# Kernel tuning notes

Measured on AMD Instinct MI355X. Metric: run time of the kernel, lower is better.

The kernel has to match this reference:

```python
import jax, jax.numpy as jnp
import numpy as np

B, N3, N4, DIM, HEADS, MLP = 256, 256, 64, 512, 8, 2048
EPS = 1e-5

def _sinusoid(n_position, d_hid):
    pos = np.arange(n_position)[:, None].astype(np.float64)
    i = np.arange(d_hid)[None, :]
    angle = pos / np.power(10000.0, 2 * (i // 2) / d_hid)
    tab = np.empty((n_position, d_hid))
    tab[:, 0::2] = np.sin(angle[:, 0::2])
    tab[:, 1::2] = np.cos(angle[:, 1::2])
    return jnp.asarray(tab[None], dtype=jnp.float32)  # [1, n, d]

def _ln(x, g, b):
    m = x.mean(-1, keepdims=True)
    v = ((x - m) ** 2).mean(-1, keepdims=True)
    return (x - m) / jnp.sqrt(v + EPS) * g + b

def setup_inputs() -> dict:
    key = jax.random.key(0)
    ks = jax.random.split(key, 12)
    s = 0.02
    d = {
        'f3': jax.random.normal(ks[0], (B, N3, DIM), jnp.float32),
        'f4': jax.random.normal(ks[1], (B, N4, DIM), jnp.float32),
        'pos3': _sinusoid(N3, DIM),
        'pos4': _sinusoid(N4, DIM),
        'ln1_g': jnp.ones((DIM,), jnp.float32), 'ln1_b': jnp.zeros((DIM,), jnp.float32),
        'ln2_g': jnp.ones((DIM,), jnp.float32), 'ln2_b': jnp.zeros((DIM,), jnp.float32),
        'ln3_g': jnp.ones((DIM,), jnp.float32), 'ln3_b': jnp.zeros((DIM,), jnp.float32),
        'Wq': jax.random.normal(ks[2], (DIM, DIM), jnp.float32) * s, 'bq': jnp.zeros((DIM,), jnp.float32),
        'Wk': jax.random.normal(ks[3], (DIM, DIM), jnp.float32) * s, 'bk': jnp.zeros((DIM,), jnp.float32),
        'Wv': jax.random.normal(ks[4], (DIM, DIM), jnp.float32) * s, 'bv': jnp.zeros((DIM,), jnp.float32),
        'Wr': jax.random.normal(ks[5], (DIM, DIM), jnp.float32) * s, 'br': jnp.zeros((DIM,), jnp.float32),
        'W1': jax.random.normal(ks[6], (DIM, MLP), jnp.float32) * s, 'b1': jnp.zeros((MLP,), jnp.float32),
        'W2': jax.random.normal(ks[7], (MLP, DIM), jnp.float32) * s, 'b2': jnp.zeros((DIM,), jnp.float32),
    }
    return d

def reference(f3, f4, pos3, pos4, ln1_g, ln1_b, ln2_g, ln2_b, ln3_g, ln3_b,
              Wq, bq, Wk, bk, Wv, bv, Wr, br, W1, b1, W2, b2):
    dk = DIM // HEADS
    f3n = _ln(f3, ln1_g, ln1_b)
    f4n = _ln(f4, ln2_g, ln2_b)
    # projections (dropout=0 -> eval mode)
    q = (f3n + pos3) @ Wq + bq  # [B,N3,D]
    k = (f4n + pos4) @ Wk + bk  # [B,N4,D]
    v = f4n @ Wv + bv           # [B,N4,D]
    # split heads along channel dim (contiguous slices == reshape with head major)
    q = q.reshape(B, N3, HEADS, dk).transpose(0, 2, 3, 1)  # [B,H,dk,N3]
    k = k.reshape(B, N4, HEADS, dk).transpose(0, 2, 3, 1)  # [B,H,dk,N4]
    v = v.reshape(B, N4, HEADS, dk).transpose(0, 2, 3, 1)  # [B,H,dv,N4]
    q = jax.nn.softmax(q, axis=2)  # softmax over head channels
    k = jax.nn.softmax(k, axis=3)  # softmax over key positions
    context = jnp.einsum('bhkn,bhvn->bhkv', k, v)          # [B,H,dk,dv]
    att = jnp.einsum('bhkv,bhkn->bhvn', context, q)        # [B,H,dv,N3]
    att = att.transpose(0, 3, 1, 2).reshape(B, N3, DIM)    # concat heads -> [B,N3,D]
    f3 = f3 + (att @ Wr + br)
    h = _ln(f3, ln3_g, ln3_b)
    h = jax.nn.gelu(h @ W1 + b1, approximate=False) @ W2 + b2
    return f3 + h
```

## Files before the change

kernel.cpp:

```cpp
#include <hip/hip_runtime.h>
#include <hip/hip_bf16.h>

typedef __attribute__((ext_vector_type(8))) short short8v;
typedef __attribute__((ext_vector_type(4))) float f32x4;
typedef __hip_bfloat16 bf16;

#define BDIM 512
#define NHEADS 8
#define DK 64
#define NBATCH 256
#define NN3 256
#define NN4 64
#define NMLP 2048

#define GLOAD_LDS16(g, l)                                                  \
  __builtin_amdgcn_global_load_lds(                                        \
      (const __attribute__((address_space(1))) void*)(g),                  \
      (__attribute__((address_space(3))) void*)(l), 16, 0, 0)

__device__ __forceinline__ float bf2f(short s) {
  union { short u[2]; float f; } cv;
  cv.u[0] = 0; cv.u[1] = s;
  return cv.f;
}
__device__ __forceinline__ short f2bf(float x) {
  bf16 h = __float2bfloat16(x);
  return *reinterpret_cast<short*>(&h);
}

__global__ __launch_bounds__(256) void convt_kernel(
    const float* __restrict__ W, bf16* __restrict__ Wt, int K, int N) {
  __shared__ float tile[32][33];
  int bx = blockIdx.x * 32, by = blockIdx.y * 32;
  int tx = threadIdx.x, ty = threadIdx.y;
#pragma unroll
  for (int j = 0; j < 32; j += 8)
    tile[ty + j][tx] = W[(size_t)(by + ty + j) * N + bx + tx];
  __syncthreads();
#pragma unroll
  for (int j = 0; j < 32; j += 8)
    Wt[(size_t)(bx + ty + j) * K + by + tx] = __float2bfloat16(tile[tx][ty + j]);
}

__global__ __launch_bounds__(256) void ln_kernel(
    const float* __restrict__ x, const float* __restrict__ g,
    const float* __restrict__ beta, const float* __restrict__ pos, int nmod,
    bf16* __restrict__ out1, bf16* __restrict__ out2, bf16* __restrict__ raw) {
  int w = threadIdx.x >> 6, lane = threadIdx.x & 63;
  int row = blockIdx.x * 4 + w;
  int c0 = lane * 8;
  const float* xr = x + (size_t)row * BDIM + c0;
  float4 v0 = *(const float4*)xr;
  float4 v1 = *(const float4*)(xr + 4);
  float f[8] = {v0.x, v0.y, v0.z, v0.w, v1.x, v1.y, v1.z, v1.w};
  float s = 0.f, sq = 0.f;
#pragma unroll
  for (int i = 0; i < 8; i++) {
    s += f[i];
    sq += f[i] * f[i];
  }
#pragma unroll
  for (int o = 1; o <= 32; o <<= 1) {
    s += __shfl_xor(s, o);
    sq += __shfl_xor(sq, o);
  }
  float mean = s * (1.f / BDIM);
  float var = sq * (1.f / BDIM) - mean * mean;
  float rstd = rsqrtf(var + 1e-5f);
  float4 g0 = *(const float4*)(g + c0);
  float4 g1 = *(const float4*)(g + c0 + 4);
  float4 b0 = *(const float4*)(beta + c0);
  float4 b1 = *(const float4*)(beta + c0 + 4);
  float gg[8] = {g0.x, g0.y, g0.z, g0.w, g1.x, g1.y, g1.z, g1.w};
  float bb[8] = {b0.x, b0.y, b0.z, b0.w, b1.x, b1.y, b1.z, b1.w};
  float pv[8] = {};
  if (pos) {
    int n = row % nmod;
    const float* pr = pos + (size_t)n * BDIM + c0;
    float4 p0 = *(const float4*)pr;
    float4 p1 = *(const float4*)(pr + 4);
    pv[0] = p0.x; pv[1] = p0.y; pv[2] = p0.z; pv[3] = p0.w;
    pv[4] = p1.x; pv[5] = p1.y; pv[6] = p1.z; pv[7] = p1.w;
  }
  short8v o1, o2, rw;
#pragma unroll
  for (int i = 0; i < 8; i++) {
    float nv = (f[i] - mean) * rstd * gg[i] + bb[i];
    o1[i] = f2bf(nv + pv[i]);
    o2[i] = f2bf(nv);
    rw[i] = f2bf(f[i]);
  }
  size_t ob = (size_t)row * BDIM + c0;
  *(short8v*)(out1 + ob) = o1;
  if (out2) *(short8v*)(out2 + ob) = o2;
  if (raw) *(short8v*)(raw + ob) = rw;
}

__global__ __launch_bounds__(256) void lnb_kernel(
    const bf16* __restrict__ x, const float* __restrict__ g,
    const float* __restrict__ beta, bf16* __restrict__ out) {
  int w = threadIdx.x >> 6, lane = threadIdx.x & 63;
  int row = blockIdx.x * 4 + w;
  int c0 = lane * 8;
  short8v v = *(const short8v*)(x + (size_t)row * BDIM + c0);
  float f[8];
  float s = 0.f, sq = 0.f;
#pragma unroll
  for (int i = 0; i < 8; i++) {
    f[i] = bf2f(v[i]);
    s += f[i];
    sq += f[i] * f[i];
  }
#pragma unroll
  for (int o = 1; o <= 32; o <<= 1) {
    s += __shfl_xor(s, o);
    sq += __shfl_xor(sq, o);
  }
  float mean = s * (1.f / BDIM);
  float var = sq * (1.f / BDIM) - mean * mean;
  float rstd = rsqrtf(var + 1e-5f);
  float4 g0 = *(const float4*)(g + c0);
  float4 g1 = *(const float4*)(g + c0 + 4);
  float4 b0 = *(const float4*)(beta + c0);
  float4 b1 = *(const float4*)(beta + c0 + 4);
  float gg[8] = {g0.x, g0.y, g0.z, g0.w, g1.x, g1.y, g1.z, g1.w};
  float bb[8] = {b0.x, b0.y, b0.z, b0.w, b1.x, b1.y, b1.z, b1.w};
  short8v o1;
#pragma unroll
  for (int i = 0; i < 8; i++) o1[i] = f2bf((f[i] - mean) * rstd * gg[i] + bb[i]);
  *(short8v*)(out + (size_t)row * BDIM + c0) = o1;
}

template <int EPI>
__global__ __launch_bounds__(512, 4) void gemm_kernel(
    const bf16* __restrict__ X, const bf16* __restrict__ Wt,
    const float* __restrict__ bias, const void* __restrict__ src, void* outp,
    int K, int ldx, int ldw, int N, int gridX) {
  extern __shared__ bf16 lds[];

  int nwg = gridDim.x;
  int cpx = nwg >> 3;
  int bid = blockIdx.x;
  int nb = (bid & 7) * cpx + (bid >> 3);
  int bx = nb % gridX, by = nb / gridX;
  int row0 = by * 128, col0 = bx * 256;

  int t = threadIdx.x, w = t >> 6, lane = t & 63;
  int wr = w >> 2, wc = w & 3;
  int r16 = lane & 15, kg = lane >> 4;
  int srow = lane >> 2;
  int scol = ((lane & 3) ^ (srow & 3)) * 8;

  const bf16* gA0 = X + (size_t)(row0 + w * 16 + srow) * ldx + scol;
  const bf16* gB0 = Wt + (size_t)(col0 + w * 32 + srow) * ldw + scol;

  f32x4 acc[4][4] = {};

  auto stage = [&](int kt, int buf) {
    bf16* base = lds + buf * 12288;
    int ke = kt << 5;
    GLOAD_LDS16(gA0 + ke, base + w * 512 + lane * 8);
    GLOAD_LDS16(gB0 + ke, base + 4096 + w * 1024 + lane * 8);
    GLOAD_LDS16(gB0 + ke + (size_t)16 * ldw,
                base + 4096 + w * 1024 + 512 + lane * 8);
  };

  auto compute = [&](int buf) {
    const char* base = (const char*)(lds + buf * 12288);
    int cc = ((kg ^ (r16 & 3)) << 4);
    short8v a[4], b[4];
#pragma unroll
    for (int m = 0; m < 4; m++)
      a[m] = *(const short8v*)(base + (wr * 64 + m * 16 + r16) * 64 + cc);
#pragma unroll
    for (int n = 0; n < 4; n++)
      b[n] = *(const short8v*)(base + 8192 + (wc * 64 + n * 16 + r16) * 64 + cc);
#pragma unroll
    for (int m = 0; m < 4; m++)
#pragma unroll
      for (int n = 0; n < 4; n++)
        acc[m][n] =
            __builtin_amdgcn_mfma_f32_16x16x32_bf16(a[m], b[n], acc[m][n], 0, 0, 0);
  };

  int NT = K >> 5;
  stage(0, 0);
  stage(1, 1);
  for (int tt = 0; tt < NT; tt++) {
    if (tt < NT - 1)
      asm volatile("s_waitcnt vmcnt(3)" ::: "memory");
    else
      asm volatile("s_waitcnt vmcnt(0)" ::: "memory");
    __builtin_amdgcn_s_barrier();
    asm volatile("" ::: "memory");
    compute(tt & 1);
    asm volatile("" ::: "memory");
    __builtin_amdgcn_s_barrier();
    asm volatile("" ::: "memory");
    if (tt + 2 < NT) stage(tt + 2, tt & 1);
  }

#pragma unroll
  for (int n = 0; n < 4; n++) {
    int col = col0 + wc * 64 + n * 16 + r16;
    float bv = bias ? bias[col] : 0.f;
#pragma unroll
    for (int m = 0; m < 4; m++)
#pragma unroll
      for (int r = 0; r < 4; r++) {
        int row = row0 + wr * 64 + m * 16 + kg * 4 + r;
        size_t o = (size_t)row * N + col;
        float val = acc[m][n][r] + bv;
        if (EPI == 0) {
          ((bf16*)outp)[o] = __float2bfloat16(val);
        } else if (EPI == 1) {
          float z = 1.5957691f * val * (1.f + 0.044715f * val * val);
          float gl = val / (1.f + __expf(-z));
          ((bf16*)outp)[o] = __float2bfloat16(gl);
        } else if (EPI == 3) {
          ((bf16*)outp)[o] = __float2bfloat16(bf2f(((const short*)src)[o]) + val);
        } else {
          ((float*)outp)[o] = bf2f(((const short*)src)[o]) + val;
        }
      }
  }
}

__global__ __launch_bounds__(256) void ctx_kernel(
    const bf16* __restrict__ kproj, const bf16* __restrict__ vbuf,
    bf16* __restrict__ ctxT) {
  int bh = blockIdx.x;
  int b = bh >> 3, h = bh & 7;
  __shared__ bf16 lk[NN4][DK], lv[NN4][DK];
  int t = threadIdx.x;
#pragma unroll
  for (int i = 0; i < 16; i++) {
    int idx = i * 256 + t;
    int n = idx >> 6, c = idx & 63;
    size_t gaddr = (size_t)b * NN4 * BDIM + (size_t)n * BDIM + h * DK + c;
    lk[n][c] = kproj[gaddr];
    lv[n][c] = vbuf[gaddr];
  }
  __syncthreads();
  if (t < 64) {
    int c = t;
    float e[NN4];
    float m = -1e30f;
#pragma unroll
    for (int n = 0; n < NN4; n++) {
      e[n] = bf2f(*(short*)&lk[n][c]);
      m = fmaxf(m, e[n]);
    }
    float s = 0.f;
#pragma unroll
    for (int n = 0; n < NN4; n++) {
      e[n] = __expf(e[n] - m);
      s += e[n];
    }
    float inv = 1.f / s;
#pragma unroll
    for (int n = 0; n < NN4; n++) lk[n][c] = __float2bfloat16(e[n] * inv);
  }
  __syncthreads();
  int vc = t >> 2;
  int kc0 = (t & 3) * 16;
  float acc[16] = {};
  for (int n = 0; n < NN4; n++) {
    float vv = __bfloat162float(lv[n][vc]);
#pragma unroll
    for (int i = 0; i < 16; i++)
      acc[i] += vv * __bfloat162float(lk[n][kc0 + i]);
  }
  size_t o = (size_t)bh * 4096 + (size_t)vc * 64 + kc0;
#pragma unroll
  for (int i = 0; i < 16; i++) ctxT[o + i] = __float2bfloat16(acc[i]);
}

__global__ __launch_bounds__(256) void att_kernel(
    const bf16* __restrict__ qproj, const bf16* __restrict__ ctxT,
    bf16* __restrict__ att) {
  int bh = blockIdx.x;
  int b = bh >> 3, h = bh & 7;
  int t = threadIdx.x, w = t >> 6, lane = t & 63;
  int r16 = lane & 15, kg = lane >> 4;
  f32x4 acc[4][4] = {};
  const bf16* qb = qproj + (size_t)b * NN3 * BDIM + h * DK;
  const bf16* cb = ctxT + (size_t)bh * 4096;
  short8v bb[2][4];
#pragma unroll
  for (int kt = 0; kt < 2; kt++)
#pragma unroll
    for (int ni = 0; ni < 4; ni++)
      bb[kt][ni] = *(const short8v*)(cb + (ni * 16 + r16) * 64 + kt * 32 + kg * 8);
#pragma unroll
  for (int mi = 0; mi < 4; mi++) {
    int rrow = w * 64 + mi * 16 + r16;
    short8v a0 = *(const short8v*)(qb + (size_t)rrow * BDIM + kg * 8);
    short8v a1 = *(const short8v*)(qb + (size_t)rrow * BDIM + 32 + kg * 8);
    float f[16];
#pragma unroll
    for (int i = 0; i < 8; i++) {
      f[i] = bf2f(a0[i]);
      f[8 + i] = bf2f(a1[i]);
    }
    float m = f[0];
#pragma unroll
    for (int i = 1; i < 16; i++) m = fmaxf(m, f[i]);
    m = fmaxf(m, __shfl_xor(m, 16));
    m = fmaxf(m, __shfl_xor(m, 32));
    float s = 0.f;
#pragma unroll
    for (int i = 0; i < 16; i++) {
      f[i] = __expf(f[i] - m);
      s += f[i];
    }
    s += __shfl_xor(s, 16);
    s += __shfl_xor(s, 32);
    float inv = 1.f / s;
    short8v A0, A1;
#pragma unroll
    for (int i = 0; i < 8; i++) {
      A0[i] = f2bf(f[i] * inv);
      A1[i] = f2bf(f[8 + i] * inv);
    }
#pragma unroll
    for (int ni = 0; ni < 4; ni++) {
      acc[mi][ni] = __builtin_amdgcn_mfma_f32_16x16x32_bf16(A0, bb[0][ni], acc[mi][ni], 0, 0, 0);
      acc[mi][ni] = __builtin_amdgcn_mfma_f32_16x16x32_bf16(A1, bb[1][ni], acc[mi][ni], 0, 0, 0);
    }
  }
#pragma unroll
  for (int mi = 0; mi < 4; mi++)
#pragma unroll
    for (int ni = 0; ni < 4; ni++)
#pragma unroll
      for (int r = 0; r < 4; r++) {
        int row = w * 64 + mi * 16 + kg * 4 + r;
        int col = ni * 16 + r16;
        att[(size_t)(b * NN3 + row) * BDIM + h * DK + col] =
            __float2bfloat16(acc[mi][ni][r]);
      }
}

extern "C" void kernel_launch(void* const* d_in, const int* in_sizes, int n_in,
                              void* d_out, int out_size, void* d_ws, size_t ws_size,
                              hipStream_t stream) {
  const float* f3 = (const float*)d_in[0];
  const float* f4 = (const float*)d_in[1];
  const float* pos3 = (const float*)d_in[2];
  const float* pos4 = (const float*)d_in[3];
  const float* ln1_g = (const float*)d_in[4];
  const float* ln1_b = (const float*)d_in[5];
  const float* ln2_g = (const float*)d_in[6];
  const float* ln2_b = (const float*)d_in[7];
  const float* ln3_g = (const float*)d_in[8];
  const float* ln3_b = (const float*)d_in[9];
  const float* Wq = (const float*)d_in[10];
  const float* bq = (const float*)d_in[11];
  const float* Wk = (const float*)d_in[12];
  const float* bk = (const float*)d_in[13];
  const float* Wv = (const float*)d_in[14];
  const float* bv = (const float*)d_in[15];
  const float* Wr = (const float*)d_in[16];
  const float* br = (const float*)d_in[17];
  const float* W1 = (const float*)d_in[18];
  const float* b1 = (const float*)d_in[19];
  const float* W2 = (const float*)d_in[20];
  const float* b2 = (const float*)d_in[21];
  float* out = (float*)d_out;

  const int M3 = NBATCH * NN3;
  const int M4 = NBATCH * NN4;
  const int MC = M3 / 2;

  char* ws = (char*)d_ws;
  size_t off = 0;
  auto alloc = [&](size_t bytes) {
    size_t r = off;
    off = (off + bytes + 255) & ~(size_t)255;
    return r;
  };
  size_t oWqt = alloc((size_t)BDIM * BDIM * 2);
  size_t oWkt = alloc((size_t)BDIM * BDIM * 2);
  size_t oWvt = alloc((size_t)BDIM * BDIM * 2);
  size_t oWrt = alloc((size_t)BDIM * BDIM * 2);
  size_t oW1t = alloc((size_t)BDIM * NMLP * 2);
  size_t oW2t = alloc((size_t)BDIM * NMLP * 2);
  size_t oXQ = alloc((size_t)M3 * BDIM * 2);
  size_t oXK = alloc((size_t)M4 * BDIM * 2);
  size_t oXV = alloc((size_t)M4 * BDIM * 2);
  size_t oQF = alloc((size_t)M3 * BDIM * 2);
  size_t oKF = alloc((size_t)M4 * BDIM * 2);
  size_t oVF = alloc((size_t)M4 * BDIM * 2);
  size_t oF3B = alloc((size_t)M3 * BDIM * 2);
  size_t oCT = alloc((size_t)NBATCH * NHEADS * DK * DK * 2);
  size_t oH1 = alloc((size_t)MC * NMLP * 2);
  (void)ws_size;

  bf16* Wqt = (bf16*)(ws + oWqt);
  bf16* Wkt = (bf16*)(ws + oWkt);
  bf16* Wvt = (bf16*)(ws + oWvt);
  bf16* Wrt = (bf16*)(ws + oWrt);
  bf16* W1t = (bf16*)(ws + oW1t);
  bf16* W2t = (bf16*)(ws + oW2t);
  bf16* XQ = (bf16*)(ws + oXQ);
  bf16* XK = (bf16*)(ws + oXK);
  bf16* XV = (bf16*)(ws + oXV);
  bf16* QF = (bf16*)(ws + oQF);
  bf16* KF = (bf16*)(ws + oKF);
  bf16* VF = (bf16*)(ws + oVF);
  bf16* F3B = (bf16*)(ws + oF3B);
  bf16* CT = (bf16*)(ws + oCT);
  bf16* H1 = (bf16*)(ws + oH1);
  bf16* ATT = XQ;
  bf16* F3O = QF;
  bf16* YN = XQ;

  hipFuncSetAttribute((const void*)gemm_kernel<0>,
                      hipFuncAttributeMaxDynamicSharedMemorySize, 49152);
  hipFuncSetAttribute((const void*)gemm_kernel<1>,
                      hipFuncAttributeMaxDynamicSharedMemorySize, 49152);
  hipFuncSetAttribute((const void*)gemm_kernel<3>,
                      hipFuncAttributeMaxDynamicSharedMemorySize, 49152);
  hipFuncSetAttribute((const void*)gemm_kernel<4>,
                      hipFuncAttributeMaxDynamicSharedMemorySize, 49152);

  convt_kernel<<<dim3(BDIM / 32, BDIM / 32), dim3(32, 8), 0, stream>>>(Wq, Wqt, BDIM, BDIM);
  convt_kernel<<<dim3(BDIM / 32, BDIM / 32), dim3(32, 8), 0, stream>>>(Wk, Wkt, BDIM, BDIM);
  convt_kernel<<<dim3(BDIM / 32, BDIM / 32), dim3(32, 8), 0, stream>>>(Wv, Wvt, BDIM, BDIM);
  convt_kernel<<<dim3(BDIM / 32, BDIM / 32), dim3(32, 8), 0, stream>>>(Wr, Wrt, BDIM, BDIM);
  convt_kernel<<<dim3(NMLP / 32, BDIM / 32), dim3(32, 8), 0, stream>>>(W1, W1t, BDIM, NMLP);
  convt_kernel<<<dim3(BDIM / 32, NMLP / 32), dim3(32, 8), 0, stream>>>(W2, W2t, NMLP, BDIM);

  ln_kernel<<<M3 / 4, 256, 0, stream>>>(f3, ln1_g, ln1_b, pos3, NN3, XQ, nullptr, F3B);
  ln_kernel<<<M4 / 4, 256, 0, stream>>>(f4, ln2_g, ln2_b, pos4, NN4, XK, XV, nullptr);

  gemm_kernel<0><<<(BDIM / 256) * (M3 / 128), 512, 49152, stream>>>(
      XQ, Wqt, bq, nullptr, QF, BDIM, BDIM, BDIM, BDIM, BDIM / 256);
  gemm_kernel<0><<<(BDIM / 256) * (M4 / 128), 512, 49152, stream>>>(
      XK, Wkt, bk, nullptr, KF, BDIM, BDIM, BDIM, BDIM, BDIM / 256);
  gemm_kernel<0><<<(BDIM / 256) * (M4 / 128), 512, 49152, stream>>>(
      XV, Wvt, bv, nullptr, VF, BDIM, BDIM, BDIM, BDIM, BDIM / 256);

  ctx_kernel<<<NBATCH * NHEADS, 256, 0, stream>>>(KF, VF, CT);
  att_kernel<<<NBATCH * NHEADS, 256, 0, stream>>>(QF, CT, ATT);

  gemm_kernel<3><<<(BDIM / 256) * (M3 / 128), 512, 49152, stream>>>(
      ATT, Wrt, br, F3B, F3O, BDIM, BDIM, BDIM, BDIM, BDIM / 256);

  lnb_kernel<<<M3 / 4, 256, 0, stream>>>(F3O, ln3_g, ln3_b, YN);

  for (int c = 0; c < 2; c++) {
    const bf16* Yc = YN + (size_t)c * MC * BDIM;
    const bf16* Fc = F3O + (size_t)c * MC * BDIM;
    float* outc = out + (size_t)c * MC * BDIM;
    gemm_kernel<1><<<(NMLP / 256) * (MC / 128), 512, 49152, stream>>>(
        Yc, W1t, b1, nullptr, H1, BDIM, BDIM, BDIM, NMLP, NMLP / 256);
    gemm_kernel<4><<<(BDIM / 256) * (MC / 128), 512, 49152, stream>>>(
        H1, W2t, b2, Fc, outc, NMLP, NMLP, NMLP, BDIM, BDIM / 256);
  }
}
```

Measured before the change: 848.0 us.

## Replace GEMM with 256x256 tile, BK=64, eight-phase interleaved load/MFMA pipeline

Swaps the 128x256-tile, BK=32 GEMM for a 256x256-tile, BK=64 kernel with 128KB double-buffered LDS. The kernel splits each k-step into four sub-phases that interleave global-to-LDS staging with MFMA work. The aim is more reuse per loaded byte and better overlap of loads with compute. The cost is fewer workgroups per CU (occupancy 2), a doubled accumulator register footprint, and half as many tiles, which may underfill the GPU on the small K/V projections.

New measurement: 806.3 us. 4.9% less time.

```diff
diff --git a/kernel.cpp b/kernel.cpp
--- a/kernel.cpp
+++ b/kernel.cpp
@@ -131,84 +131,111 @@
   *(short8v*)(out + (size_t)row * BDIM + c0) = o1;
 }
 
+#define VM4 asm volatile("s_waitcnt vmcnt(4)" ::: "memory")
+#define VM2 asm volatile("s_waitcnt vmcnt(2)" ::: "memory")
+#define VM0 asm volatile("s_waitcnt vmcnt(0)" ::: "memory")
+#define BARR                          \
+  __builtin_amdgcn_s_barrier();       \
+  asm volatile("" ::: "memory")
+
+#define PH_A(SLOT, MH)                                                        \
+  _Pragma("unroll") for (int mq = 0; mq < 4; mq++) {                          \
+    _Pragma("unroll") for (int ks = 0; ks < 2; ks++) {                        \
+      int rl = wr * 64 + mq * 16 + r16;                                       \
+      ac[mq][ks] = *(const short8v*)((const char*)lds + (SLOT)*65536 +        \
+          (MH)*16384 + rl * 128 + ((((ks << 2) + kg) ^ (rl & 7)) << 4));      \
+    }                                                                          \
+  }
+#define PH_B(SLOT, NH)                                                        \
+  _Pragma("unroll") for (int nq = 0; nq < 2; nq++) {                          \
+    _Pragma("unroll") for (int ks = 0; ks < 2; ks++) {                        \
+      int cl = wc * 16 + nq * 64 + r16;                                       \
+      bb[nq][ks] = *(const short8v*)((const char*)lds + (SLOT)*65536 +        \
+          32768 + (NH)*16384 + cl * 128 + ((((ks << 2) + kg) ^ (cl & 7)) << 4)); \
+    }                                                                          \
+  }
+#define PH_MMA(MH, NH)                                                        \
+  _Pragma("unroll") for (int mq = 0; mq < 4; mq++)                            \
+  _Pragma("unroll") for (int nq = 0; nq < 2; nq++)                            \
+  _Pragma("unroll") for (int ks = 0; ks < 2; ks++)                            \
+    acc[(MH)*4 + mq][(NH)*2 + nq] = __builtin_amdgcn_mfma_f32_16x16x32_bf16(  \
+        ac[mq][ks], bb[nq][ks], acc[(MH)*4 + mq][(NH)*2 + nq], 0, 0, 0);
+
 template <int EPI>
-__global__ __launch_bounds__(512, 4) void gemm_kernel(
+__global__ __launch_bounds__(512, 2) void gemm8p_kernel(
     const bf16* __restrict__ X, const bf16* __restrict__ Wt,
     const float* __restrict__ bias, const void* __restrict__ src, void* outp,
     int K, int ldx, int ldw, int N, int gridX) {
   extern __shared__ bf16 lds[];
 
-  int nwg = gridDim.x;
-  int cpx = nwg >> 3;
-  int bid = blockIdx.x;
+  int nwg = gridDim.x, cpx = nwg >> 3, bid = blockIdx.x;
   int nb = (bid & 7) * cpx + (bid >> 3);
   int bx = nb % gridX, by = nb / gridX;
-  int row0 = by * 128, col0 = bx * 256;
+  int row0 = by * 256, col0 = bx * 256;
 
   int t = threadIdx.x, w = t >> 6, lane = t & 63;
   int wr = w >> 2, wc = w & 3;
   int r16 = lane & 15, kg = lane >> 4;
-  int srow = lane >> 2;
-  int scol = ((lane & 3) ^ (srow & 3)) * 8;
-
-  const bf16* gA0 = X + (size_t)(row0 + w * 16 + srow) * ldx + scol;
-  const bf16* gB0 = Wt + (size_t)(col0 + w * 32 + srow) * ldw + scol;
-
-  f32x4 acc[4][4] = {};
-
-  auto stage = [&](int kt, int buf) {
-    bf16* base = lds + buf * 12288;
-    int ke = kt << 5;
-    GLOAD_LDS16(gA0 + ke, base + w * 512 + lane * 8);
-    GLOAD_LDS16(gB0 + ke, base + 4096 + w * 1024 + lane * 8);
-    GLOAD_LDS16(gB0 + ke + (size_t)16 * ldw,
-                base + 4096 + w * 1024 + 512 + lane * 8);
+
+  int srow = t >> 3, ssl = t & 7;
+  int scol = (ssl ^ (srow & 7)) * 8;
+  const bf16* gA = X + (size_t)(row0 + srow) * ldx + scol;
+  const bf16* gB = Wt + (size_t)(col0 + srow) * ldw + scol;
+
+  f32x4 acc[8][4] = {};
+  short8v ac[4][2], bb[2][2];
+
+  auto stageA = [&](int kt, int u, int slot) {
+    bf16* d = lds + slot * 32768 + u * 8192 + t * 8;
+    const bf16* s = gA + (size_t)(u * 128) * ldx + (kt << 6);
+    GLOAD_LDS16(s, d);
+    GLOAD_LDS16(s + (size_t)64 * ldx, d + 4096);
   };
-
-  auto compute = [&](int buf) {
-    const char* base = (const char*)(lds + buf * 12288);
-    int cc = ((kg ^ (r16 & 3)) << 4);
-    short8v a[4], b[4];
-#pragma unroll
-    for (int m = 0; m < 4; m++)
-      a[m] = *(const short8v*)(base + (wr * 64 + m * 16 + r16) * 64 + cc);
-#pragma unroll
-    for (int n = 0; n < 4; n++)
-      b[n] = *(const short8v*)(base + 8192 + (wc * 64 + n * 16 + r16) * 64 + cc);
-#pragma unroll
-    for (int m = 0; m < 4; m++)
-#pragma unroll
-      for (int n = 0; n < 4; n++)
-        acc[m][n] =
-            __builtin_amdgcn_mfma_f32_16x16x32_bf16(a[m], b[n], acc[m][n], 0, 0, 0);
+  auto stageB = [&](int kt, int u, int slot) {
+    bf16* d = lds + slot * 32768 + 16384 + u * 8192 + t * 8;
+    const bf16* s = gB + (size_t)(u * 128) * ldw + (kt << 6);
+    GLOAD_LDS16(s, d);
+    GLOAD_LDS16(s + (size_t)64 * ldw, d + 4096);
   };
 
-  int NT = K >> 5;
-  stage(0, 0);
-  stage(1, 1);
-  for (int tt = 0; tt < NT; tt++) {
-    if (tt < NT - 1)
-      asm volatile("s_waitcnt vmcnt(3)" ::: "memory");
-    else
-      asm volatile("s_waitcnt vmcnt(0)" ::: "memory");
-    __builtin_amdgcn_s_barrier();
-    asm volatile("" ::: "memory");
-    compute(tt & 1);
-    asm volatile("" ::: "memory");
-    __builtin_amdgcn_s_barrier();
-    asm volatile("" ::: "memory");
-    if (tt + 2 < NT) stage(tt + 2, tt & 1);
+  int NT = K >> 6;
+  stageA(0, 0, 0);
+  stageB(0, 0, 0);
+  stageB(0, 1, 0);
+  stageA(0, 1, 0);
+
+  for (int tt = 0; tt < NT - 1; tt++) {
+    int sl = tt & 1, sn = sl ^ 1;
+    VM4; BARR;
+    stageA(tt + 1, 0, sn);
+    PH_A(sl, 0); PH_B(sl, 0); PH_MMA(0, 0);
+    VM4; BARR;
+    stageB(tt + 1, 0, sn);
+    PH_B(sl, 1); PH_MMA(0, 1);
+    VM4; BARR;
+    stageB(tt + 1, 1, sn);
+    PH_A(sl, 1); PH_B(sl, 0); PH_MMA(1, 0);
+    BARR;
+    stageA(tt + 1, 1, sn);
+    PH_B(sl, 1); PH_MMA(1, 1);
+  }
+  {
+    int sl = (NT - 1) & 1;
+    VM4; BARR; PH_A(sl, 0); PH_B(sl, 0); PH_MMA(0, 0);
+    VM2; BARR; PH_B(sl, 1); PH_MMA(0, 1);
+    VM0; BARR; PH_A(sl, 1); PH_B(sl, 0); PH_MMA(1, 0);
+    BARR;      PH_B(sl, 1); PH_MMA(1, 1);
   }
 
 #pragma unroll
   for (int n = 0; n < 4; n++) {
-    int col = col0 + wc * 64 + n * 16 + r16;
+    int col = col0 + (n & 1) * 64 + (n >> 1) * 128 + wc * 16 + r16;
     float bv = bias ? bias[col] : 0.f;
 #pragma unroll
-    for (int m = 0; m < 4; m++)
+    for (int m = 0; m < 8; m++)
 #pragma unroll
       for (int r = 0; r < 4; r++) {
-        int row = row0 + wr * 64 + m * 16 + kg * 4 + r;
+        int row = row0 + wr * 64 + (m & 3) * 16 + (m >> 2) * 128 + kg * 4 + r;
         size_t o = (size_t)row * N + col;
         float val = acc[m][n][r] + bv;
         if (EPI == 0) {
@@ -286,12 +313,12 @@
   f32x4 acc[4][4] = {};
   const bf16* qb = qproj + (size_t)b * NN3 * BDIM + h * DK;
   const bf16* cb = ctxT + (size_t)bh * 4096;
-  short8v bb[2][4];
+  short8v bbv[2][4];
 #pragma unroll
   for (int kt = 0; kt < 2; kt++)
 #pragma unroll
     for (int ni = 0; ni < 4; ni++)
-      bb[kt][ni] = *(const short8v*)(cb + (ni * 16 + r16) * 64 + kt * 32 + kg * 8);
+      bbv[kt][ni] = *(const short8v*)(cb + (ni * 16 + r16) * 64 + kt * 32 + kg * 8);
 #pragma unroll
   for (int mi = 0; mi < 4; mi++) {
     int rrow = w * 64 + mi * 16 + r16;
@@ -325,8 +352,8 @@
     }
 #pragma unroll
     for (int ni = 0; ni < 4; ni++) {
-      acc[mi][ni] = __builtin_amdgcn_mfma_f32_16x16x32_bf16(A0, bb[0][ni], acc[mi][ni], 0, 0, 0);
-      acc[mi][ni] = __builtin_amdgcn_mfma_f32_16x16x32_bf16(A1, bb[1][ni], acc[mi][ni], 0, 0, 0);
+      acc[mi][ni] = __builtin_amdgcn_mfma_f32_16x16x32_bf16(A0, bbv[0][ni], acc[mi][ni], 0, 0, 0);
+      acc[mi][ni] = __builtin_amdgcn_mfma_f32_16x16x32_bf16(A1, bbv[1][ni], acc[mi][ni], 0, 0, 0);
     }
   }
 #pragma unroll
@@ -416,14 +443,14 @@
   bf16* F3O = QF;
   bf16* YN = XQ;
 
-  hipFuncSetAttribute((const void*)gemm_kernel<0>,
-                      hipFuncAttributeMaxDynamicSharedMemorySize, 49152);
-  hipFuncSetAttribute((const void*)gemm_kernel<1>,
-                      hipFuncAttributeMaxDynamicSharedMemorySize, 49152);
-  hipFuncSetAttribute((const void*)gemm_kernel<3>,
-                      hipFuncAttributeMaxDynamicSharedMemorySize, 49152);
-  hipFuncSetAttribute((const void*)gemm_kernel<4>,
-                      hipFuncAttributeMaxDynamicSharedMemorySize, 49152);
+  hipFuncSetAttribute((const void*)gemm8p_kernel<0>,
+                      hipFuncAttributeMaxDynamicSharedMemorySize, 131072);
+  hipFuncSetAttribute((const void*)gemm8p_kernel<1>,
+                      hipFuncAttributeMaxDynamicSharedMemorySize, 131072);
+  hipFuncSetAttribute((const void*)gemm8p_kernel<3>,
+                      hipFuncAttributeMaxDynamicSharedMemorySize, 131072);
+  hipFuncSetAttribute((const void*)gemm8p_kernel<4>,
+                      hipFuncAttributeMaxDynamicSharedMemorySize, 131072);
 
   convt_kernel<<<dim3(BDIM / 32, BDIM / 32), dim3(32, 8), 0, stream>>>(Wq, Wqt, BDIM, BDIM);
   convt_kernel<<<dim3(BDIM / 32, BDIM / 32), dim3(32, 8), 0, stream>>>(Wk, Wkt, BDIM, BDIM);
@@ -435,17 +462,17 @@
   ln_kernel<<<M3 / 4, 256, 0, stream>>>(f3, ln1_g, ln1_b, pos3, NN3, XQ, nullptr, F3B);
   ln_kernel<<<M4 / 4, 256, 0, stream>>>(f4, ln2_g, ln2_b, pos4, NN4, XK, XV, nullptr);
 
-  gemm_kernel<0><<<(BDIM / 256) * (M3 / 128), 512, 49152, stream>>>(
+  gemm8p_kernel<0><<<(BDIM / 256) * (M3 / 256), 512, 131072, stream>>>(
       XQ, Wqt, bq, nullptr, QF, BDIM, BDIM, BDIM, BDIM, BDIM / 256);
-  gemm_kernel<0><<<(BDIM / 256) * (M4 / 128), 512, 49152, stream>>>(
+  gemm8p_kernel<0><<<(BDIM / 256) * (M4 / 256), 512, 131072, stream>>>(
       XK, Wkt, bk, nullptr, KF, BDIM, BDIM, BDIM, BDIM, BDIM / 256);
-  gemm_kernel<0><<<(BDIM / 256) * (M4 / 128), 512, 49152, stream>>>(
+  gemm8p_kernel<0><<<(BDIM / 256) * (M4 / 256), 512, 131072, stream>>>(
       XV, Wvt, bv, nullptr, VF, BDIM, BDIM, BDIM, BDIM, BDIM / 256);
 
   ctx_kernel<<<NBATCH * NHEADS, 256, 0, stream>>>(KF, VF, CT);
   att_kernel<<<NBATCH * NHEADS, 256, 0, stream>>>(QF, CT, ATT);
 
-  gemm_kernel<3><<<(BDIM / 256) * (M3 / 128), 512, 49152, stream>>>(
+  gemm8p_kernel<3><<<(BDIM / 256) * (M3 / 256), 512, 131072, stream>>>(
       ATT, Wrt, br, F3B, F3O, BDIM, BDIM, BDIM, BDIM, BDIM / 256);
 
   lnb_kernel<<<M3 / 4, 256, 0, stream>>>(F3O, ln3_g, ln3_b, YN);
@@ -454,9 +481,9 @@
     const bf16* Yc = YN + (size_t)c * MC * BDIM;
     const bf16* Fc = F3O + (size_t)c * MC * BDIM;
     float* outc = out + (size_t)c * MC * BDIM;
-    gemm_kernel<1><<<(NMLP / 256) * (MC / 128), 512, 49152, stream>>>(
+    gemm8p_kernel<1><<<(NMLP / 256) * (MC / 256), 512, 131072, stream>>>(
         Yc, W1t, b1, nullptr, H1, BDIM, BDIM, BDIM, NMLP, NMLP / 256);
-    gemm_kernel<4><<<(BDIM / 256) * (MC / 128), 512, 49152, stream>>>(
+    gemm8p_kernel<4><<<(BDIM / 256) * (MC / 256), 512, 131072, stream>>>(
         H1, W2t, b2, Fc, outc, NMLP, NMLP, NMLP, BDIM, BDIM / 256);
   }
 }
```
